# Optimization experiments

Measured on AMD Instinct MI355X. Metric: run time of the kernel, lower is better.

Reference implementation:

```python
import jax, jax.numpy as jnp
import numpy as np

N_NODES = 20000
SEQ_T = 24
EMB = 64
H_LSTM = 128
H_GCN = 128
OUT = 16
N_CAT = 20000
N_EDGE = 640000


def setup_inputs() -> dict:
    key = jax.random.key(0)
    ks = jax.random.split(key, 16)
    s = 0.05
    emb = jax.random.normal(ks[4], (N_CAT + 1, EMB), jnp.float32) * s
    emb = emb.at[0].set(0.0)  # padding_idx=0
    inp = {
        "x_tokens": jax.random.randint(ks[0], (N_NODES, SEQ_T), 0, N_CAT + 1, dtype=jnp.int32),
        "lengths": jax.random.randint(ks[1], (N_NODES,), 1, SEQ_T + 1, dtype=jnp.int32),
        "edge_index": jax.random.randint(ks[2], (2, N_EDGE), 0, N_NODES, dtype=jnp.int32),
        "edge_weight": jax.random.uniform(ks[3], (N_EDGE,), jnp.float32, 0.1, 1.0),
        "emb": emb,
        "W_ih": jax.random.normal(ks[5], (4 * H_LSTM, EMB), jnp.float32) * s,
        "W_hh": jax.random.normal(ks[6], (4 * H_LSTM, H_LSTM), jnp.float32) * s,
        "b_ih": jax.random.normal(ks[7], (4 * H_LSTM,), jnp.float32) * s,
        "b_hh": jax.random.normal(ks[8], (4 * H_LSTM,), jnp.float32) * s,
        "conv1_W": jax.random.normal(ks[9], (H_LSTM, H_GCN), jnp.float32) * s,
        "conv1_b": jax.random.normal(ks[10], (H_GCN,), jnp.float32) * s,
        "conv2_W": jax.random.normal(ks[11], (H_GCN, H_GCN), jnp.float32) * s,
        "conv2_b": jax.random.normal(ks[12], (H_GCN,), jnp.float32) * s,
        "fc_W": jax.random.normal(ks[13], (H_GCN, OUT), jnp.float32) * s,
        "fc_b": jax.random.normal(ks[14], (OUT,), jnp.float32) * s,
    }
    return inp


def _lstm_last(xseq, lengths, W_ih, W_hh, b):
    # xseq: [N, T, E]; unidirectional LSTM -> output at t=len-1 equals
    # pack_padded_sequence result (causality). PyTorch gate order: i, f, g, o.
    n = xseq.shape[0]
    h0 = jnp.zeros((n, H_LSTM), xseq.dtype)

    def step(carry, xt):
        h, c = carry
        z = xt @ W_ih.T + h @ W_hh.T + b  # [N, 4H]
        i, f, g, o = jnp.split(z, 4, axis=-1)
        c = jax.nn.sigmoid(f) * c + jax.nn.sigmoid(i) * jnp.tanh(g)
        h = jax.nn.sigmoid(o) * jnp.tanh(c)
        return (h, c), h

    _, hs = jax.lax.scan(step, (h0, h0), jnp.swapaxes(xseq, 0, 1))  # hs: [T, N, H]
    return hs[lengths - 1, jnp.arange(n)]  # [N, H]


def _gcn_conv(x, W, b, src, dst, w, n):
    # PyG GCNConv: self loops (weight 1) + symmetric normalization.
    h = x @ W  # [N, G]
    deg = jax.ops.segment_sum(w, dst, num_segments=n) + 1.0
    dinv = jax.lax.rsqrt(deg)
    norm = dinv[src] * w * dinv[dst]  # [E]
    agg = jax.ops.segment_sum(h[src] * norm[:, None], dst, num_segments=n)
    agg = agg + h * (dinv * dinv)[:, None]  # self-loop term
    return agg + b


def reference(x_tokens, lengths, edge_index, edge_weight, emb, W_ih, W_hh,
              b_ih, b_hh, conv1_W, conv1_b, conv2_W, conv2_b, fc_W, fc_b):
    n = x_tokens.shape[0]
    src, dst = edge_index[0], edge_index[1]
    xe = emb[x_tokens]  # [N, T, E]
    x = _lstm_last(xe, lengths, W_ih, W_hh, b_ih + b_hh)  # [N, H_LSTM]
    x = jax.nn.relu(_gcn_conv(x, conv1_W, conv1_b, src, dst, edge_weight, n))
    # dropout: identity (eval mode)
    x = jax.nn.relu(_gcn_conv(x, conv2_W, conv2_b, src, dst, edge_weight, n))
    return x @ fc_W + fc_b  # [N, OUT]
```

## Files before the change

kernel.cpp:

```cpp
#include <hip/hip_runtime.h>
#include <math.h>

#define N_NODES 20000
#define SEQ_T   24
#define EMBD    64
#define HL      128
#define OUTF    16
#define NEDGE   640000
#define G4      512
#define KTOT    192
#define ROWS    80
#define RF      5
#define NBLSTM  250
#define LDA     232
#define WSTRIDE 12288

#define NBCSR   250
#define EPB     (NEDGE/NBCSR)
#define NPB     (N_NODES/NBCSR)
#define CSRT    1024

#define CROWS   64
#define CRF     4
#define NCBLK   313
#define CPAD    136

typedef __bf16 bf16x8 __attribute__((ext_vector_type(8)));
typedef __bf16 bf16x2 __attribute__((ext_vector_type(2)));
typedef float  f32x4  __attribute__((ext_vector_type(4)));

__device__ __forceinline__ float4 ld4(const float* p){ return *reinterpret_cast<const float4*>(p); }
__device__ __forceinline__ void st4(float* p, float4 v){ *reinterpret_cast<float4*>(p) = v; }

#define LOG2E 1.44269504f

#define S_EMB   320016
#define S_WTP   (S_EMB + KTOT*G4)
#define S_C1    (S_WTP + 16384)
#define S_C2    (S_C1 + 16384)
#define S_BIAS  (S_C2 + G4)
#define PREPBLK ((S_BIAS + 255)/256)

__global__ __launch_bounds__(256) void prep_all(
    const float* __restrict__ emb,  __bf16* __restrict__ embb,
    const float* __restrict__ Wih,  const float* __restrict__ Whh,
    __bf16* __restrict__ WTp,
    const float* __restrict__ c1W,  __bf16* __restrict__ wc1b,
    const float* __restrict__ c2W,  __bf16* __restrict__ wc2b,
    const float* __restrict__ bi,   const float* __restrict__ bh,
    float* __restrict__ bs)
{
    int gid = blockIdx.x*256 + threadIdx.x;
    if (gid < S_EMB) {
        int i4 = gid*4;
        float4 v = ld4(emb + i4);
        embb[i4+0] = (__bf16)v.x;
        embb[i4+1] = (__bf16)v.y;
        embb[i4+2] = (__bf16)v.z;
        embb[i4+3] = (__bf16)v.w;
    } else if (gid < S_WTP) {
        int idx = gid - S_EMB;
        int ko = idx & 31;
        int c  = (idx >> 5) & 15;
        int gt = (idx >> 9) & 3;
        int kc = (idx >> 11) % 6;
        int w  = idx / WSTRIDE;
        int g  = gt*HL + w*16 + c;
        int kk = kc*32 + ko;
        float v = (kk < EMBD) ? Wih[g*EMBD + kk] : Whh[g*HL + (kk - EMBD)];
        WTp[idx] = (__bf16)v;
    } else if (gid < S_C2) {
        bool c2 = (gid >= S_C1);
        int idx = gid - (c2 ? S_C1 : S_WTP);
        const float* W = c2 ? c2W : c1W;
        __bf16* dst = c2 ? wc2b : wc1b;
        int ko = idx & 31;
        int c  = (idx >> 5) & 15;
        int kc = (idx >> 9) & 3;
        int w  = idx >> 11;
        int g  = w*16 + c;
        int k  = kc*32 + ko;
        dst[idx] = (__bf16)W[k*HL + g];
    } else if (gid < S_BIAS) {
        int i = gid - S_C2;
        bs[i] = bi[i] + bh[i];
    }
}

__global__ __launch_bounds__(CSRT) void csr_count(
    const int* __restrict__ esrc, const int* __restrict__ edst,
    const float* __restrict__ ew,
    int* __restrict__ rank, int* __restrict__ gcnt, float* __restrict__ gdeg)
{
    __shared__ int   hist[N_NODES];
    __shared__ float fdeg[N_NODES];
    const int tid = threadIdx.x, bid = blockIdx.x;
    const int e0 = bid * EPB;

    uint4* h4 = reinterpret_cast<uint4*>(hist);
    uint4* f4 = reinterpret_cast<uint4*>(fdeg);
    for (int i = tid; i < N_NODES/4; i += CSRT) {
        h4[i] = make_uint4(0,0,0,0);
        f4[i] = make_uint4(0,0,0,0);
    }
    __syncthreads();

    #pragma unroll
    for (int k = 0; k < 3; ++k) {
        int i = tid + CSRT*k;
        if (k < 2 || i < EPB) {
            int e = e0 + i;
            int d = edst[e];
            rank[e] = atomicAdd(&hist[d], 1);
            atomicAdd(&fdeg[d], ew[e]);
        }
    }
    __syncthreads();

    for (int i = tid; i < N_NODES; i += CSRT) {
        gcnt[(size_t)bid*N_NODES + i] = hist[i];
        gdeg[(size_t)bid*N_NODES + i] = fdeg[i];
    }
}

__global__ __launch_bounds__(CSRT) void csr_scan(
    int* __restrict__ gcnt, const float* __restrict__ gdeg,
    float* __restrict__ dinv, int* __restrict__ tot)
{
    __shared__ int   ctile[NBCSR*NPB];
    __shared__ float dtile[NBCSR*NPB];
    const int tid = threadIdx.x, bid = blockIdx.x;
    const int nodes0 = bid * NPB;

    for (int idx = tid; idx < NBCSR*NPB; idx += CSRT) {
        int b = idx / NPB, i = idx - b*NPB;
        ctile[idx] = gcnt[(size_t)b*N_NODES + nodes0 + i];
        dtile[idx] = gdeg[(size_t)b*N_NODES + nodes0 + i];
    }
    __syncthreads();
    if (tid < NPB) {
        int run = 0; float dsum = 0.f;
        for (int b = 0; b < NBCSR; ++b) {
            int v = ctile[b*NPB + tid];
            ctile[b*NPB + tid] = run;
            run += v;
            dsum += dtile[b*NPB + tid];
        }
        tot[nodes0 + tid]  = run;
        dinv[nodes0 + tid] = rsqrtf(dsum + 1.0f);
    }
    __syncthreads();
    for (int idx = tid; idx < NBCSR*NPB; idx += CSRT) {
        int b = idx / NPB, i = idx - b*NPB;
        gcnt[(size_t)b*N_NODES + nodes0 + i] = ctile[idx];
    }
}

__global__ __launch_bounds__(256) void csr_rowstart(const int* __restrict__ tot,
                                                    int* __restrict__ row_start)
{
    __shared__ int part[NBCSR];
    const int t = threadIdx.x;
    if (t < NBCSR) {
        int s = 0;
        for (int i = 0; i < NPB; ++i) s += tot[t*NPB + i];
        part[t] = s;
    }
    __syncthreads();
    if (t == 0) {
        int run = 0;
        for (int b = 0; b < NBCSR; ++b) { int v = part[b]; part[b] = run; run += v; }
    }
    __syncthreads();
    if (t < NBCSR) {
        int base = part[t];
        for (int i = 0; i < NPB; ++i) {
            row_start[t*NPB + i] = base;
            base += tot[t*NPB + i];
        }
        if (t == NBCSR - 1) row_start[N_NODES] = base;
    }
}

__global__ __launch_bounds__(CSRT) void csr_fill(
    const int* __restrict__ esrc, const int* __restrict__ edst,
    const float* __restrict__ ew,
    const int* __restrict__ rank, const int* __restrict__ gcnt,
    const int* __restrict__ row_start, const float* __restrict__ dinv,
    int* __restrict__ src_s, float* __restrict__ norm_s)
{
    const int tid = threadIdx.x, bid = blockIdx.x;
    const int e0 = bid * EPB;
    #pragma unroll
    for (int k = 0; k < 3; ++k) {
        int i = tid + CSRT*k;
        if (k < 2 || i < EPB) {
            int e = e0 + i;
            int d = edst[e], s = esrc[e];
            int pos = row_start[d] + gcnt[(size_t)bid*N_NODES + d] + rank[e];
            src_s[pos]  = s;
            norm_s[pos] = dinv[s] * ew[e] * dinv[d];
        }
    }
}

__global__ __launch_bounds__(512, 2) void lstm_fused(
    const int* __restrict__ tokens, const int* __restrict__ lengths,
    const __bf16* __restrict__ embb, const __bf16* __restrict__ WTp,
    const float* __restrict__ bsum, float* __restrict__ hlast)
{
    __shared__ __align__(16) __bf16 a_lds[ROWS][LDA];
    __shared__ int tok_lds[ROWS*SEQ_T];
    __shared__ int len_lds[ROWS];

    const int tid = threadIdx.x;
    const int n0  = blockIdx.x * ROWS;
    const int w   = tid >> 6;
    const int l   = tid & 63;
    const int l15 = l & 15, l4 = l >> 4;

    #pragma unroll
    for (int i = 0; i < 4; ++i) {
        int idx = tid + 512*i;
        if (idx < ROWS*SEQ_T) tok_lds[idx] = tokens[n0*SEQ_T + idx];
    }
    if (tid < ROWS) len_lds[tid] = lengths[n0 + tid];

    #pragma unroll
    for (int i = 0; i < 3; ++i) {
        int idx = tid + 512*i;
        if (idx < ROWS*16) {
            int row = idx >> 4, s = idx & 15;
            *reinterpret_cast<uint4*>(&a_lds[row][EMBD + s*8]) = make_uint4(0,0,0,0);
        }
    }

    float bias_v[4];
    #pragma unroll
    for (int gt = 0; gt < 4; ++gt)
        bias_v[gt] = bsum[gt*HL + w*16 + l15];

    bf16x8 wreg[6][4];
    {
        const __bf16* wbase = WTp + (size_t)w * WSTRIDE;
        #pragma unroll
        for (int kc = 0; kc < 6; ++kc)
            #pragma unroll
            for (int gt = 0; gt < 4; ++gt)
                wreg[kc][gt] = *reinterpret_cast<const bf16x8*>(
                    &wbase[(size_t)(((kc*4 + gt)*16 + l15)*32) + l4*8]);
    }

    f32x4 acc[RF][4];
    float c_reg[RF][4];
    {
        f32x4 zz = {0.f,0.f,0.f,0.f};
        #pragma unroll
        for (int rf = 0; rf < RF; ++rf) {
            #pragma unroll
            for (int gt = 0; gt < 4; ++gt) acc[rf][gt] = zz;
            #pragma unroll
            for (int r = 0; r < 4; ++r) c_reg[rf][r] = 0.f;
        }
    }

    for (int t = 0; t < SEQ_T; ++t) {
        #pragma unroll
        for (int i = 0; i < 2; ++i) {
            int idx = tid + 512*i;
            if (idx < ROWS*8) {
                int row = idx >> 3, sl = idx & 7;
                int tok = tok_lds[row*SEQ_T + t];
                *reinterpret_cast<uint4*>(&a_lds[row][sl*8]) =
                    *reinterpret_cast<const uint4*>(&embb[(size_t)tok*EMBD + sl*8]);
            }
        }
        __syncthreads();

        #pragma unroll
        for (int kc = 0; kc < 6; ++kc)
            #pragma unroll
            for (int rf = 0; rf < RF; ++rf) {
                bf16x8 af = *reinterpret_cast<const bf16x8*>(
                    &a_lds[rf*16 + l15][kc*32 + l4*8]);
                #pragma unroll
                for (int gt = 0; gt < 4; ++gt)
                    acc[rf][gt] = __builtin_amdgcn_mfma_f32_16x16x32_bf16(
                        af, wreg[kc][gt], acc[rf][gt], 0, 0, 0);
            }
        __syncthreads();

        #pragma unroll
        for (int rf = 0; rf < RF; ++rf) {
            f32x4 zi4 = acc[rf][0], zf4 = acc[rf][1];
            f32x4 zg4 = acc[rf][2], zo4 = acc[rf][3];
            #pragma unroll
            for (int r = 0; r < 4; ++r) {
                int row = rf*16 + l4*4 + r;
                float zi = zi4[r] + bias_v[0];
                float zf = zf4[r] + bias_v[1];
                float zg = zg4[r] + bias_v[2];
                float zo = zo4[r] + bias_v[3];
                float ef = __builtin_amdgcn_exp2f(-LOG2E*zf);
                float ei = __builtin_amdgcn_exp2f(-LOG2E*zi);
                float eg = __builtin_amdgcn_exp2f(2.0f*LOG2E*zg);
                float sf  = __builtin_amdgcn_rcpf(1.0f + ef);
                float rig = __builtin_amdgcn_rcpf((1.0f + ei)*(eg + 1.0f));
                float cc = sf*c_reg[rf][r] + (eg - 1.0f)*rig;
                c_reg[rf][r] = cc;
                float eo = __builtin_amdgcn_exp2f(-LOG2E*zo);
                float ec = __builtin_amdgcn_exp2f(2.0f*LOG2E*cc);
                float rh = __builtin_amdgcn_rcpf((1.0f + eo)*(ec + 1.0f));
                float h = (ec - 1.0f)*rh;
                int j = w*16 + l15;
                a_lds[row][EMBD + j] = (__bf16)h;
                if (len_lds[row] == t + 1)
                    __builtin_nontemporal_store(h, &hlast[(size_t)(n0 + row)*HL + j]);
            }
            f32x4 zz = {0.f,0.f,0.f,0.f};
            acc[rf][0] = zz; acc[rf][1] = zz; acc[rf][2] = zz; acc[rf][3] = zz;
        }
    }
}

template<bool BF16IN>
__global__ __launch_bounds__(512) void gemm_mfma(const void* __restrict__ xin,
                                                 const __bf16* __restrict__ Wb,
                                                 __bf16* __restrict__ y, int N)
{
    __shared__ __align__(16) __bf16 a_lds[CROWS][CPAD];
    const int tid = threadIdx.x;
    const int n0 = blockIdx.x * CROWS;
    const int w = tid >> 6, l = tid & 63;
    const int l15 = l & 15, l4 = l >> 4;

    {
        int row = tid >> 3, sl = tid & 7;
        int n = n0 + row;
        if (BF16IN) {
            const __bf16* xb = (const __bf16*)xin;
            uint4 v0 = make_uint4(0,0,0,0), v1 = make_uint4(0,0,0,0);
            if (n < N) {
                v0 = *reinterpret_cast<const uint4*>(xb + (size_t)n*HL + sl*16);
                v1 = *reinterpret_cast<const uint4*>(xb + (size_t)n*HL + sl*16 + 8);
            }
            *reinterpret_cast<uint4*>(&a_lds[row][sl*16])     = v0;
            *reinterpret_cast<uint4*>(&a_lds[row][sl*16 + 8]) = v1;
        } else {
            const float* x = (const float*)xin;
            __bf16 tmp[16];
            if (n < N) {
                #pragma unroll
                for (int q = 0; q < 4; ++q) {
                    float4 v = ld4(x + (size_t)n*HL + sl*16 + q*4);
                    tmp[q*4+0] = (__bf16)v.x; tmp[q*4+1] = (__bf16)v.y;
                    tmp[q*4+2] = (__bf16)v.z; tmp[q*4+3] = (__bf16)v.w;
                }
            } else {
                #pragma unroll
                for (int q = 0; q < 16; ++q) tmp[q] = (__bf16)0.f;
            }
            *reinterpret_cast<uint4*>(&a_lds[row][sl*16])     = *reinterpret_cast<uint4*>(&tmp[0]);
            *reinterpret_cast<uint4*>(&a_lds[row][sl*16 + 8]) = *reinterpret_cast<uint4*>(&tmp[8]);
        }
    }

    bf16x8 wb[4];
    #pragma unroll
    for (int kc = 0; kc < 4; ++kc)
        wb[kc] = *reinterpret_cast<const bf16x8*>(
            &Wb[(size_t)(((w*4 + kc)*16 + l15)*32) + l4*8]);

    f32x4 acc[CRF];
    {
        f32x4 zz = {0.f,0.f,0.f,0.f};
        #pragma unroll
        for (int rf = 0; rf < CRF; ++rf) acc[rf] = zz;
    }
    __syncthreads();

    #pragma unroll
    for (int kc = 0; kc < 4; ++kc)
        #pragma unroll
        for (int rf = 0; rf < CRF; ++rf) {
            bf16x8 af = *reinterpret_cast<const bf16x8*>(
                &a_lds[rf*16 + l15][kc*32 + l4*8]);
            acc[rf] = __builtin_amdgcn_mfma_f32_16x16x32_bf16(af, wb[kc], acc[rf], 0, 0, 0);
        }

    int j = w*16 + l15;
    #pragma unroll
    for (int rf = 0; rf < CRF; ++rf)
        #pragma unroll
        for (int r = 0; r < 4; ++r) {
            int n = n0 + rf*16 + l4*4 + r;
            if (n < N) y[(size_t)n*HL + j] = (__bf16)acc[rf][r];
        }
}

template<int MODE>
__global__ __launch_bounds__(256) void gcn_gather_k(
    const int* __restrict__ row_start, const int* __restrict__ src_s,
    const float* __restrict__ norm_s, const float* __restrict__ dinv,
    const __bf16* __restrict__ y, const float* __restrict__ b,
    __bf16* __restrict__ outb,
    const float* __restrict__ fcW, const float* __restrict__ fcb,
    float* __restrict__ fcout, int N)
{
    __shared__ float xrow[4][HL];
    const int tid = threadIdx.x;
    int gt = blockIdx.x*256 + tid;
    int n = gt >> 6, lane = gt & 63;
    bool act = (n < N);
    float ax = 0.f, ay = 0.f;
    if (act) {
        const int beg = row_start[n], end = row_start[n+1];
        int p = beg;
        for (; p + 4 <= end; p += 4) {
            int   s0 = src_s[p+0], s1 = src_s[p+1], s2 = src_s[p+2], s3 = src_s[p+3];
            float w0 = norm_s[p+0], w1 = norm_s[p+1], w2 = norm_s[p+2], w3 = norm_s[p+3];
            bf16x2 v0 = *reinterpret_cast<const bf16x2*>(y + (size_t)s0*HL + lane*2);
            bf16x2 v1 = *reinterpret_cast<const bf16x2*>(y + (size_t)s1*HL + lane*2);
            bf16x2 v2 = *reinterpret_cast<const bf16x2*>(y + (size_t)s2*HL + lane*2);
            bf16x2 v3 = *reinterpret_cast<const bf16x2*>(y + (size_t)s3*HL + lane*2);
            ax = fmaf(w0, (float)v0[0], ax); ay = fmaf(w0, (float)v0[1], ay);
            ax = fmaf(w1, (float)v1[0], ax); ay = fmaf(w1, (float)v1[1], ay);
            ax = fmaf(w2, (float)v2[0], ax); ay = fmaf(w2, (float)v2[1], ay);
            ax = fmaf(w3, (float)v3[0], ax); ay = fmaf(w3, (float)v3[1], ay);
        }
        for (; p < end; ++p) {
            int s = src_s[p];
            float nrm = norm_s[p];
            bf16x2 v = *reinterpret_cast<const bf16x2*>(y + (size_t)s*HL + lane*2);
            ax = fmaf(nrm, (float)v[0], ax);
            ay = fmaf(nrm, (float)v[1], ay);
        }
        float di = dinv[n];
        float sl = di*di;
        bf16x2 vs = *reinterpret_cast<const bf16x2*>(y + (size_t)n*HL + lane*2);
        ax = fmaf(sl, (float)vs[0], ax);
        ay = fmaf(sl, (float)vs[1], ay);
        float2 bb = *reinterpret_cast<const float2*>(b + lane*2);
        ax = fmaxf(ax + bb.x, 0.f);
        ay = fmaxf(ay + bb.y, 0.f);
    }
    if (MODE == 1) {
        if (act) {
            bf16x2 o;
            o[0] = (__bf16)ax; o[1] = (__bf16)ay;
            *reinterpret_cast<bf16x2*>(outb + (size_t)n*HL + lane*2) = o;
        }
    } else {
        int nq = tid >> 6;
        xrow[nq][lane*2]     = ax;
        xrow[nq][lane*2 + 1] = ay;
        __syncthreads();
        if (tid < 64) {
            int q = tid >> 4, o = tid & 15;
            int nn = blockIdx.x*4 + q;
            if (nn < N) {
                float a = fcb[o];
                #pragma unroll 8
                for (int k = 0; k < HL; ++k)
                    a = fmaf(xrow[q][k], fcW[k*OUTF + o], a);
                fcout[(size_t)nn*OUTF + o] = a;
            }
        }
    }
}

extern "C" void kernel_launch(void* const* d_in, const int* in_sizes, int n_in,
                              void* d_out, int out_size, void* d_ws, size_t ws_size,
                              hipStream_t stream)
{
    const int*   x_tokens = (const int*)d_in[0];
    const int*   lengths  = (const int*)d_in[1];
    const int*   eidx     = (const int*)d_in[2];
    const float* ew       = (const float*)d_in[3];
    const float* emb      = (const float*)d_in[4];
    const float* W_ih     = (const float*)d_in[5];
    const float* W_hh     = (const float*)d_in[6];
    const float* b_ih     = (const float*)d_in[7];
    const float* b_hh     = (const float*)d_in[8];
    const float* c1W      = (const float*)d_in[9];
    const float* c1b      = (const float*)d_in[10];
    const float* c2W      = (const float*)d_in[11];
    const float* c2b      = (const float*)d_in[12];
    const float* fcW      = (const float*)d_in[13];
    const float* fcb      = (const float*)d_in[14];
    float* out = (float*)d_out;

    const int* esrc = eidx;
    const int* edst = eidx + NEDGE;

    char* ws = (char*)d_ws;
    size_t off = 0;
    auto take = [&](size_t bytes) -> char* {
        char* p = ws + off;
        off = (off + bytes + 255) & ~(size_t)255;
        return p;
    };
    const size_t NH = (size_t)N_NODES * HL * sizeof(float);
    __bf16* embb = (__bf16*)take((size_t)(N_NODES + 1) * EMBD * sizeof(__bf16));
    __bf16* WTp  = (__bf16*)take((size_t)KTOT * G4 * sizeof(__bf16));
    __bf16* wc1b = (__bf16*)take((size_t)HL * HL * sizeof(__bf16));
    __bf16* wc2b = (__bf16*)take((size_t)HL * HL * sizeof(__bf16));
    float* bsum  = (float*)take((size_t)G4 * sizeof(float));
    float* hLst  = (float*)take(NH);
    __bf16* ybf  = (__bf16*)take((size_t)N_NODES * HL * sizeof(__bf16));
    __bf16* x2b  = (__bf16*)take((size_t)N_NODES * HL * sizeof(__bf16));
    float* dinvb = (float*)take((size_t)N_NODES * sizeof(float));
    int*   rankb = (int*)  take((size_t)NEDGE * sizeof(int));
    int*   gcnt  = (int*)  take((size_t)NBCSR * N_NODES * sizeof(int));
    float* gdeg  = (float*)take((size_t)NBCSR * N_NODES * sizeof(float));
    int*   totb  = (int*)  take((size_t)N_NODES * sizeof(int));
    int*   rowst = (int*)  take((size_t)(N_NODES + 1) * sizeof(int));
    int*   srcS  = (int*)  take((size_t)NEDGE * sizeof(int));
    float* nrmS  = (float*)take((size_t)NEDGE * sizeof(float));

    prep_all<<<PREPBLK, 256, 0, stream>>>(emb, embb, W_ih, W_hh, WTp,
                                          c1W, wc1b, c2W, wc2b, b_ih, b_hh, bsum);

    csr_count<<<NBCSR, CSRT, 0, stream>>>(esrc, edst, ew, rankb, gcnt, gdeg);
    csr_scan<<<NBCSR, CSRT, 0, stream>>>(gcnt, gdeg, dinvb, totb);
    csr_rowstart<<<1, 256, 0, stream>>>(totb, rowst);
    csr_fill<<<NBCSR, CSRT, 0, stream>>>(esrc, edst, ew, rankb, gcnt, rowst,
                                         dinvb, srcS, nrmS);

    lstm_fused<<<NBLSTM, 512, 0, stream>>>(x_tokens, lengths, embb, WTp, bsum, hLst);

    const int gathBlocks = (N_NODES*64 + 255)/256;

    gemm_mfma<false><<<NCBLK, 512, 0, stream>>>(hLst, wc1b, ybf, N_NODES);
    gcn_gather_k<1><<<gathBlocks, 256, 0, stream>>>(rowst, srcS, nrmS, dinvb, ybf,
                                                    c1b, x2b, nullptr, nullptr, nullptr, N_NODES);
    gemm_mfma<true><<<NCBLK, 512, 0, stream>>>(x2b, wc2b, ybf, N_NODES);
    gcn_gather_k<2><<<gathBlocks, 256, 0, stream>>>(rowst, srcS, nrmS, dinvb, ybf,
                                                    c2b, nullptr, fcW, fcb, out, N_NODES);
}
```

Measured before the change: 299.6 us.

## Fuse first GCN linear layer into LSTM epilogue and shrink CSR counts to u16

```diff
diff --git a/kernel.cpp b/kernel.cpp
--- a/kernel.cpp
+++ b/kernel.cpp
@@ -28,6 +28,7 @@
 typedef __bf16 bf16x8 __attribute__((ext_vector_type(8)));
 typedef __bf16 bf16x2 __attribute__((ext_vector_type(2)));
 typedef float  f32x4  __attribute__((ext_vector_type(4)));
+typedef unsigned short u16;
 
 __device__ __forceinline__ float4 ld4(const float* p){ return *reinterpret_cast<const float4*>(p); }
 __device__ __forceinline__ void st4(float* p, float4 v){ *reinterpret_cast<float4*>(p) = v; }
@@ -90,7 +91,7 @@
 __global__ __launch_bounds__(CSRT) void csr_count(
     const int* __restrict__ esrc, const int* __restrict__ edst,
     const float* __restrict__ ew,
-    int* __restrict__ rank, int* __restrict__ gcnt, float* __restrict__ gdeg)
+    int* __restrict__ rank, u16* __restrict__ gcnt, float* __restrict__ gdeg)
 {
     __shared__ int   hist[N_NODES];
     __shared__ float fdeg[N_NODES];
@@ -118,16 +119,16 @@
     __syncthreads();
 
     for (int i = tid; i < N_NODES; i += CSRT) {
-        gcnt[(size_t)bid*N_NODES + i] = hist[i];
+        gcnt[(size_t)bid*N_NODES + i] = (u16)hist[i];
         gdeg[(size_t)bid*N_NODES + i] = fdeg[i];
     }
 }
 
 __global__ __launch_bounds__(CSRT) void csr_scan(
-    int* __restrict__ gcnt, const float* __restrict__ gdeg,
+    u16* __restrict__ gcnt, const float* __restrict__ gdeg,
     float* __restrict__ dinv, int* __restrict__ tot)
 {
-    __shared__ int   ctile[NBCSR*NPB];
+    __shared__ u16   ctile[NBCSR*NPB];
     __shared__ float dtile[NBCSR*NPB];
     const int tid = threadIdx.x, bid = blockIdx.x;
     const int nodes0 = bid * NPB;
@@ -142,7 +143,7 @@
         int run = 0; float dsum = 0.f;
         for (int b = 0; b < NBCSR; ++b) {
             int v = ctile[b*NPB + tid];
-            ctile[b*NPB + tid] = run;
+            ctile[b*NPB + tid] = (u16)run;
             run += v;
             dsum += dtile[b*NPB + tid];
         }
@@ -185,7 +186,7 @@
 __global__ __launch_bounds__(CSRT) void csr_fill(
     const int* __restrict__ esrc, const int* __restrict__ edst,
     const float* __restrict__ ew,
-    const int* __restrict__ rank, const int* __restrict__ gcnt,
+    const int* __restrict__ rank, const u16* __restrict__ gcnt,
     const int* __restrict__ row_start, const float* __restrict__ dinv,
     int* __restrict__ src_s, float* __restrict__ norm_s)
 {
@@ -197,7 +198,7 @@
         if (k < 2 || i < EPB) {
             int e = e0 + i;
             int d = edst[e], s = esrc[e];
-            int pos = row_start[d] + gcnt[(size_t)bid*N_NODES + d] + rank[e];
+            int pos = row_start[d] + (int)gcnt[(size_t)bid*N_NODES + d] + rank[e];
             src_s[pos]  = s;
             norm_s[pos] = dinv[s] * ew[e] * dinv[d];
         }
@@ -207,9 +208,11 @@
 __global__ __launch_bounds__(512, 2) void lstm_fused(
     const int* __restrict__ tokens, const int* __restrict__ lengths,
     const __bf16* __restrict__ embb, const __bf16* __restrict__ WTp,
-    const float* __restrict__ bsum, float* __restrict__ hlast)
+    const float* __restrict__ bsum, const __bf16* __restrict__ wc1b,
+    __bf16* __restrict__ ybf)
 {
     __shared__ __align__(16) __bf16 a_lds[ROWS][LDA];
+    __shared__ __align__(16) __bf16 hl_lds[ROWS][CPAD];
     __shared__ int tok_lds[ROWS*SEQ_T];
     __shared__ int len_lds[ROWS];
 
@@ -315,16 +318,39 @@
                 int j = w*16 + l15;
                 a_lds[row][EMBD + j] = (__bf16)h;
                 if (len_lds[row] == t + 1)
-                    __builtin_nontemporal_store(h, &hlast[(size_t)(n0 + row)*HL + j]);
+                    hl_lds[row][j] = (__bf16)h;
             }
             f32x4 zz = {0.f,0.f,0.f,0.f};
             acc[rf][0] = zz; acc[rf][1] = zz; acc[rf][2] = zz; acc[rf][3] = zz;
         }
     }
-}
-
-template<bool BF16IN>
-__global__ __launch_bounds__(512) void gemm_mfma(const void* __restrict__ xin,
+
+    __syncthreads();
+
+    {
+        bf16x8 wb1[4];
+        #pragma unroll
+        for (int kc = 0; kc < 4; ++kc)
+            wb1[kc] = *reinterpret_cast<const bf16x8*>(
+                &wc1b[(size_t)(((w*4 + kc)*16 + l15)*32) + l4*8]);
+        int j = w*16 + l15;
+        #pragma unroll
+        for (int rf = 0; rf < RF; ++rf) {
+            f32x4 a2 = {0.f,0.f,0.f,0.f};
+            #pragma unroll
+            for (int kc = 0; kc < 4; ++kc) {
+                bf16x8 af = *reinterpret_cast<const bf16x8*>(
+                    &hl_lds[rf*16 + l15][kc*32 + l4*8]);
+                a2 = __builtin_amdgcn_mfma_f32_16x16x32_bf16(af, wb1[kc], a2, 0, 0, 0);
+            }
+            #pragma unroll
+            for (int r = 0; r < 4; ++r)
+                ybf[(size_t)(n0 + rf*16 + l4*4 + r)*HL + j] = (__bf16)a2[r];
+        }
+    }
+}
+
+__global__ __launch_bounds__(512) void gemm_mfma(const __bf16* __restrict__ xb,
                                                  const __bf16* __restrict__ Wb,
                                                  __bf16* __restrict__ y, int N)
 {
@@ -337,32 +363,13 @@
     {
         int row = tid >> 3, sl = tid & 7;
         int n = n0 + row;
-        if (BF16IN) {
-            const __bf16* xb = (const __bf16*)xin;
-            uint4 v0 = make_uint4(0,0,0,0), v1 = make_uint4(0,0,0,0);
-            if (n < N) {
-                v0 = *reinterpret_cast<const uint4*>(xb + (size_t)n*HL + sl*16);
-                v1 = *reinterpret_cast<const uint4*>(xb + (size_t)n*HL + sl*16 + 8);
-            }
-            *reinterpret_cast<uint4*>(&a_lds[row][sl*16])     = v0;
-            *reinterpret_cast<uint4*>(&a_lds[row][sl*16 + 8]) = v1;
-        } else {
-            const float* x = (const float*)xin;
-            __bf16 tmp[16];
-            if (n < N) {
-                #pragma unroll
-                for (int q = 0; q < 4; ++q) {
-                    float4 v = ld4(x + (size_t)n*HL + sl*16 + q*4);
-                    tmp[q*4+0] = (__bf16)v.x; tmp[q*4+1] = (__bf16)v.y;
-                    tmp[q*4+2] = (__bf16)v.z; tmp[q*4+3] = (__bf16)v.w;
-                }
-            } else {
-                #pragma unroll
-                for (int q = 0; q < 16; ++q) tmp[q] = (__bf16)0.f;
-            }
-            *reinterpret_cast<uint4*>(&a_lds[row][sl*16])     = *reinterpret_cast<uint4*>(&tmp[0]);
-            *reinterpret_cast<uint4*>(&a_lds[row][sl*16 + 8]) = *reinterpret_cast<uint4*>(&tmp[8]);
-        }
+        uint4 v0 = make_uint4(0,0,0,0), v1 = make_uint4(0,0,0,0);
+        if (n < N) {
+            v0 = *reinterpret_cast<const uint4*>(xb + (size_t)n*HL + sl*16);
+            v1 = *reinterpret_cast<const uint4*>(xb + (size_t)n*HL + sl*16 + 8);
+        }
+        *reinterpret_cast<uint4*>(&a_lds[row][sl*16])     = v0;
+        *reinterpret_cast<uint4*>(&a_lds[row][sl*16 + 8]) = v1;
     }
 
     bf16x8 wb[4];
@@ -500,18 +507,16 @@
         off = (off + bytes + 255) & ~(size_t)255;
         return p;
     };
-    const size_t NH = (size_t)N_NODES * HL * sizeof(float);
     __bf16* embb = (__bf16*)take((size_t)(N_NODES + 1) * EMBD * sizeof(__bf16));
     __bf16* WTp  = (__bf16*)take((size_t)KTOT * G4 * sizeof(__bf16));
     __bf16* wc1b = (__bf16*)take((size_t)HL * HL * sizeof(__bf16));
     __bf16* wc2b = (__bf16*)take((size_t)HL * HL * sizeof(__bf16));
     float* bsum  = (float*)take((size_t)G4 * sizeof(float));
-    float* hLst  = (float*)take(NH);
     __bf16* ybf  = (__bf16*)take((size_t)N_NODES * HL * sizeof(__bf16));
     __bf16* x2b  = (__bf16*)take((size_t)N_NODES * HL * sizeof(__bf16));
     float* dinvb = (float*)take((size_t)N_NODES * sizeof(float));
     int*   rankb = (int*)  take((size_t)NEDGE * sizeof(int));
-    int*   gcnt  = (int*)  take((size_t)NBCSR * N_NODES * sizeof(int));
+    u16*   gcnt  = (u16*)  take((size_t)NBCSR * N_NODES * sizeof(u16));
     float* gdeg  = (float*)take((size_t)NBCSR * N_NODES * sizeof(float));
     int*   totb  = (int*)  take((size_t)N_NODES * sizeof(int));
     int*   rowst = (int*)  take((size_t)(N_NODES + 1) * sizeof(int));
@@ -527,14 +532,14 @@
     csr_fill<<<NBCSR, CSRT, 0, stream>>>(esrc, edst, ew, rankb, gcnt, rowst,
                                          dinvb, srcS, nrmS);
 
-    lstm_fused<<<NBLSTM, 512, 0, stream>>>(x_tokens, lengths, embb, WTp, bsum, hLst);
+    lstm_fused<<<NBLSTM, 512, 0, stream>>>(x_tokens, lengths, embb, WTp, bsum,
+                                           wc1b, ybf);
 
     const int gathBlocks = (N_NODES*64 + 255)/256;
 
-    gemm_mfma<false><<<NCBLK, 512, 0, stream>>>(hLst, wc1b, ybf, N_NODES);
     gcn_gather_k<1><<<gathBlocks, 256, 0, stream>>>(rowst, srcS, nrmS, dinvb, ybf,
                                                     c1b, x2b, nullptr, nullptr, nullptr, N_NODES);
-    gemm_mfma<true><<<NCBLK, 512, 0, stream>>>(x2b, wc2b, ybf, N_NODES);
+    gemm_mfma<<<NCBLK, 512, 0, stream>>>(x2b, wc2b, ybf, N_NODES);
     gcn_gather_k<2><<<gathBlocks, 256, 0, stream>>>(rowst, srcS, nrmS, dinvb, ybf,
                                                     c2b, nullptr, fcW, fcb, out, N_NODES);
 }
```

Result: faster. 286.8 us (-4.3%).
